# Performance work log

Measured on AMD Instinct MI355X. Metric: run time of the kernel, lower is better.

## Reference

```python
import math
import jax, jax.numpy as jnp
import numpy as np

B, N, C = 2, 2048, 1024
H = 16
D = C // H  # 64
LN_EPS = 1e-5


def setup_inputs() -> dict:
    key = jax.random.key(0)
    ks = jax.random.split(key, 5)
    x = jax.random.normal(ks[0], (B, N, C), dtype=jnp.float32)
    w_qkv = jax.random.normal(ks[1], (C, 3 * C), dtype=jnp.float32) * 0.02
    w_proj = jax.random.normal(ks[2], (C, C), dtype=jnp.float32) * 0.02
    b_proj = jnp.zeros((C,), dtype=jnp.float32)
    ln_w = jnp.ones((D,), dtype=jnp.float32) + jax.random.normal(ks[3], (D,), dtype=jnp.float32) * 0.02
    ln_b = jax.random.normal(ks[4], (D,), dtype=jnp.float32) * 0.02
    return {"x": x, "w_qkv": w_qkv, "w_proj": w_proj, "b_proj": b_proj,
            "ln_w": ln_w, "ln_b": ln_b}


def _layernorm(t, w, b):
    mu = jnp.mean(t, axis=-1, keepdims=True)
    var = jnp.var(t, axis=-1, keepdims=True)
    return (t - mu) * jax.lax.rsqrt(var + LN_EPS) * w + b


def reference(x, w_qkv, w_proj, b_proj, ln_w, ln_b):
    b, n, c = x.shape
    h, d = H, c // H
    # QKV projection (no bias): [b,n,3c] -> [3,b,h,n,d]
    qkv = (x @ w_qkv).reshape(b, n, 3, h, d).transpose(2, 0, 3, 1, 4)
    q, k, v = qkv[0], qkv[1], qkv[2]
    # per-head LayerNorm on q and k (qk_norm)
    q = _layernorm(q, ln_w, ln_b)
    k = _layernorm(k, ln_w, ln_b)
    # NOTE: source multiplies q by sqrt(head_dim) (faithful to original)
    q = q * jnp.asarray(math.sqrt(d), dtype=q.dtype)
    scores = jnp.einsum('bhnd,bhmd->bhnm', q, k)  # [b,h,n,n]
    mask_value = -jnp.finfo(scores.dtype).max
    causal = jnp.tril(jnp.ones((n, n), dtype=bool))
    scores = jnp.where(causal, scores, mask_value)
    attn = jax.nn.softmax(scores, axis=-1)
    out = jnp.einsum('bhnm,bhmd->bhnd', attn, v)  # [b,h,n,d]
    out = out.transpose(0, 2, 1, 3).reshape(b, n, c)  # b n (h d)
    return out @ w_proj + b_proj
```

## Files before the change

kernel.cpp:

```cpp
#include <hip/hip_runtime.h>

#define LOG2E 1.4426950408889634f

typedef _Float16 f16x8_t __attribute__((ext_vector_type(8)));
typedef _Float16 f16x4_t __attribute__((ext_vector_type(4)));
typedef _Float16 f16x2_t __attribute__((ext_vector_type(2)));
typedef float    f32x4_t __attribute__((ext_vector_type(4)));

#define MFMA32(a, b, c) __builtin_amdgcn_mfma_f32_16x16x32_f16(a, b, c, 0, 0, 0)
#define MFMA16(a, b, c) __builtin_amdgcn_mfma_f32_16x16x16f16(a, b, c, 0, 0, 0)

__device__ __forceinline__ void async_copy16(void* lds, const void* g) {
    __builtin_amdgcn_global_load_lds(
        (const __attribute__((address_space(1))) unsigned char*)g,
        (__attribute__((address_space(3))) unsigned char*)lds, 16, 0, 0);
}

__global__ void prep_k(const float* __restrict__ x, _Float16* __restrict__ xh,
                       const float* __restrict__ wq, _Float16* __restrict__ wqT,
                       const float* __restrict__ wp, _Float16* __restrict__ wpT) {
    __shared__ _Float16 tl[64][65];
    const int bx = blockIdx.x, t = threadIdx.x;
    if (bx < 4096) {
        const int i = bx * 256 + t;
        float4 v = ((const float4*)x)[i];
        f16x4_t o = { (_Float16)v.x, (_Float16)v.y, (_Float16)v.z, (_Float16)v.w };
        ((f16x4_t*)xh)[i] = o;
        return;
    }
    const float* in; _Float16* out; int C, bxx, byy;
    if (bx < 4864) { const int id = bx - 4096; in = wq; out = wqT; C = 3072; bxx = id % 48; byy = id / 48; }
    else           { const int id = bx - 4864; in = wp; out = wpT; C = 1024; bxx = id % 16; byy = id / 16; }
    const int R = 1024;
    const int c = t & 63;
    const int r4 = t >> 6;
    const int r0 = byy * 64, c0 = bxx * 64;
#pragma unroll
    for (int i = 0; i < 16; ++i) {
        int r = r4 + i * 4;
        tl[c][r] = (_Float16)in[(size_t)(r0 + r) * C + c0 + c];
    }
    __syncthreads();
#pragma unroll
    for (int i = 0; i < 16; ++i) {
        int rr = r4 + i * 4;
        out[(size_t)(c0 + rr) * R + r0 + c] = tl[rr][c];
    }
}

template <typename OutT, bool BIAS, bool LNQK>
__global__ __launch_bounds__(256, 3)
void gemm_f16_k(const _Float16* __restrict__ A, const _Float16* __restrict__ BT,
                OutT* __restrict__ C, const float* __restrict__ bias,
                _Float16* __restrict__ VTg,
                const float* __restrict__ ln_w, const float* __restrict__ ln_b,
                int M, int N, int K) {
    __shared__ _Float16 As[2][128][32];
    __shared__ _Float16 Bs[2][128][32];
    const int tid = threadIdx.x;
    const int wid = tid >> 6, lane = tid & 63;
    const int qd = lane >> 4, ln = lane & 15;
    const int m0 = blockIdx.x * 128, n0 = blockIdx.y * 128;
    const int wm = (wid >> 1) * 64, wn = (wid & 1) * 64;

    f32x4_t acc[4][4] = {};

    const int srow = lane >> 2;
    const int skk  = (lane & 3) * 8;

    for (int k0 = 0; k0 < K; k0 += 64) {
        __syncthreads();
#pragma unroll
        for (int p = 0; p < 4; ++p) {
            const int seg = p * 4 + wid;
            const int s   = seg >> 3;
            const int rg  = seg & 7;
            const int row = rg * 16 + srow;
            const size_t goff = (size_t)row * K + k0 + s * 32 + skk;
            async_copy16(&As[0][0][0] + seg * 512, A  + (size_t)m0 * K + goff);
            async_copy16(&Bs[0][0][0] + seg * 512, BT + (size_t)n0 * K + goff);
        }
        __syncthreads();
#pragma unroll
        for (int s = 0; s < 2; ++s) {
            f16x8_t a[4], b[4];
#pragma unroll
            for (int i = 0; i < 4; ++i)
                a[i] = *(const f16x8_t*)&As[s][wm + i * 16 + ln][qd * 8];
#pragma unroll
            for (int j = 0; j < 4; ++j)
                b[j] = *(const f16x8_t*)&Bs[s][wn + j * 16 + ln][qd * 8];
#pragma unroll
            for (int i = 0; i < 4; ++i)
#pragma unroll
                for (int j = 0; j < 4; ++j)
                    acc[i][j] = MFMA32(a[i], b[j], acc[i][j]);
        }
    }

    if constexpr (LNQK) {
        if (n0 >= 2048) {
            __syncthreads();
            const int h2  = ((n0 - 2048) >> 6) + (wn >> 6);
            const int row0 = m0 + wm;
            const int bb  = row0 >> 11;
            const int tt  = (row0 & 2047) >> 6;
            const size_t obase = ((size_t)(bb * 16 + h2)) * 131072 + (size_t)tt * 4096;
            _Float16* tlw = &As[0][0][0] + wid * 1088;
#pragma unroll
            for (int j = 0; j < 4; ++j) {
#pragma unroll
                for (int i = 0; i < 4; ++i) {
                    f16x4_t v;
#pragma unroll
                    for (int r = 0; r < 4; ++r) v[r] = (_Float16)acc[i][j][r];
                    *(f16x4_t*)&tlw[ln * 68 + i * 16 + qd * 4] = v;
                }
#pragma unroll
                for (int e = 0; e < 2; ++e) {
                    const int ci = lane * 2 + e;
                    const int dl = ci >> 3, w2 = ci & 7;
                    const int pq = w2 ^ (dl & 7);
                    const int base = (pq >> 2) * 32 + (pq & 3) * 4;
                    f16x4_t v0 = *(const f16x4_t*)&tlw[dl * 68 + base];
                    f16x4_t v1 = *(const f16x4_t*)&tlw[dl * 68 + base + 16];
                    f16x8_t val = __builtin_shufflevector(v0, v1, 0, 1, 2, 3, 4, 5, 6, 7);
                    *(f16x8_t*)&VTg[obase + (size_t)((j * 16 + dl) * 8 + w2) * 8] = val;
                }
            }
            return;
        }
        {
            const float scale = (n0 < 1024) ? 8.0f * LOG2E : 1.0f;
            float lw[4], lb[4];
#pragma unroll
            for (int j = 0; j < 4; ++j) { lw[j] = ln_w[j * 16 + ln]; lb[j] = ln_b[j * 16 + ln]; }
#pragma unroll
            for (int i = 0; i < 4; ++i)
#pragma unroll
                for (int r = 0; r < 4; ++r) {
                    float s = acc[i][0][r] + acc[i][1][r] + acc[i][2][r] + acc[i][3][r];
                    s += __shfl_xor(s, 1); s += __shfl_xor(s, 2);
                    s += __shfl_xor(s, 4); s += __shfl_xor(s, 8);
                    const float mu = s * 0.015625f;
                    const float d0 = acc[i][0][r] - mu, d1 = acc[i][1][r] - mu;
                    const float d2 = acc[i][2][r] - mu, d3 = acc[i][3][r] - mu;
                    float v = d0 * d0 + d1 * d1 + d2 * d2 + d3 * d3;
                    v += __shfl_xor(v, 1); v += __shfl_xor(v, 2);
                    v += __shfl_xor(v, 4); v += __shfl_xor(v, 8);
                    const float rs = rsqrtf(v * 0.015625f + 1e-5f);
                    acc[i][0][r] = (d0 * rs * lw[0] + lb[0]) * scale;
                    acc[i][1][r] = (d1 * rs * lw[1] + lb[1]) * scale;
                    acc[i][2][r] = (d2 * rs * lw[2] + lb[2]) * scale;
                    acc[i][3][r] = (d3 * rs * lw[3] + lb[3]) * scale;
                }
        }
    }

#pragma unroll
    for (int i = 0; i < 4; ++i)
#pragma unroll
        for (int j = 0; j < 4; ++j) {
            const int col = n0 + wn + j * 16 + ln;
            const float bv = BIAS ? bias[col] : 0.0f;
#pragma unroll
            for (int r = 0; r < 4; ++r) {
                const int row = m0 + wm + i * 16 + qd * 4 + r;
                C[(size_t)row * N + col] = (OutT)(acc[i][j][r] + bv);
            }
        }
}

__global__ __launch_bounds__(256, 2)
void gemm_f16_m64_k(const _Float16* __restrict__ A, const _Float16* __restrict__ BT,
                    float* __restrict__ C, const float* __restrict__ bias,
                    int M, int N, int K) {
    __shared__ _Float16 As[2][64][32];
    __shared__ _Float16 Bs[2][128][32];
    const int tid = threadIdx.x;
    const int wid = tid >> 6, lane = tid & 63;
    const int qd = lane >> 4, ln = lane & 15;
    const int m0 = blockIdx.x * 64, n0 = blockIdx.y * 128;
    const int wn = wid * 32;

    f32x4_t acc[4][2] = {};
    const int srow = lane >> 2;
    const int skk  = (lane & 3) * 8;

    for (int k0 = 0; k0 < K; k0 += 64) {
        __syncthreads();
#pragma unroll
        for (int p = 0; p < 2; ++p) {
            const int seg = p * 4 + wid;
            const int hidx = seg * 512 + lane * 8;
            const int s_ = hidx >> 11;
            const int row = (hidx >> 5) & 63;
            const int kk = hidx & 31;
            async_copy16(&As[0][0][0] + seg * 512,
                         A + (size_t)(m0 + row) * K + k0 + s_ * 32 + kk);
        }
#pragma unroll
        for (int p = 0; p < 4; ++p) {
            const int seg = p * 4 + wid;
            const int s   = seg >> 3;
            const int rg  = seg & 7;
            const int row = rg * 16 + srow;
            async_copy16(&Bs[0][0][0] + seg * 512,
                         BT + (size_t)(n0 + row) * K + k0 + s * 32 + skk);
        }
        __syncthreads();
#pragma unroll
        for (int s = 0; s < 2; ++s) {
            f16x8_t a[4], b[2];
#pragma unroll
            for (int i = 0; i < 4; ++i)
                a[i] = *(const f16x8_t*)&As[s][i * 16 + ln][qd * 8];
#pragma unroll
            for (int j = 0; j < 2; ++j)
                b[j] = *(const f16x8_t*)&Bs[s][wn + j * 16 + ln][qd * 8];
#pragma unroll
            for (int i = 0; i < 4; ++i)
#pragma unroll
                for (int j = 0; j < 2; ++j)
                    acc[i][j] = MFMA32(a[i], b[j], acc[i][j]);
        }
    }
#pragma unroll
    for (int i = 0; i < 4; ++i)
#pragma unroll
        for (int j = 0; j < 2; ++j) {
            const int col = n0 + wn + j * 16 + ln;
            const float bv = bias[col];
#pragma unroll
            for (int r = 0; r < 4; ++r) {
                const int row = m0 + i * 16 + qd * 4 + r;
                C[(size_t)row * N + col] = acc[i][j][r] + bv;
            }
        }
}

__global__ __launch_bounds__(256, 3)
void attn_part_k(const _Float16* __restrict__ qkv, const _Float16* __restrict__ VTg,
                 _Float16* __restrict__ O, float* __restrict__ Op, float* __restrict__ ml) {
    __shared__ _Float16 Ks[3][2][64][32];
    __shared__ _Float16 VT[3][64][64];

    const int tid = threadIdx.x;
    const int wid = tid >> 6, lane = tid & 63;
    const int qd = lane >> 4, ln = lane & 15;
    const int bh = blockIdx.x;
    const int b = bh >> 4, h = bh & 15;
    const int y = blockIdx.y;
    int band, chunk, nst;
    if (y < 8)       { band = 8 + y;  chunk = 0; nst = 16; }
    else if (y < 16) { band = 23 - y; chunk = 1; nst = 2 * band - 14; }
    else             { band = y - 16; chunk = 0; nst = 2 * band + 2; }
    const size_t vtbase = (size_t)bh * 131072;
    const int qrow0 = band * 128 + wid * 32;
    const int kvbeg = chunk * 1024;

    f16x8_t qf[2][2];
#pragma unroll
    for (int qt = 0; qt < 2; ++qt)
#pragma unroll
        for (int s = 0; s < 2; ++s)
            qf[qt][s] = *(const f16x8_t*)&qkv[(size_t)(b * 2048 + qrow0 + qt * 16 + ln) * 3072
                                             + h * 64 + s * 32 + qd * 8];

    f32x4_t o[2][4] = {};
    f32x4_t ls[2] = {};
    float m[2] = { -3.0e38f, -3.0e38f };
    const f16x4_t ones = { (_Float16)1.0f, (_Float16)1.0f, (_Float16)1.0f, (_Float16)1.0f };

    auto stage = [&](int buf, int kv0) {
#pragma unroll
        for (int p = 0; p < 2; ++p) {
            const int seg = p * 4 + wid;
            const int hidx = seg * 512 + lane * 8;
            const int s_ = hidx >> 11;
            const int rrow = (hidx >> 5) & 63;
            const int kk = hidx & 31;
            async_copy16(&Ks[buf][0][0][0] + seg * 512,
                         qkv + (size_t)(b * 2048 + kv0 + rrow) * 3072 + 1024 + h * 64
                             + s_ * 32 + kk);
        }
#pragma unroll
        for (int p = 0; p < 2; ++p) {
            const int seg = p * 4 + wid;
            async_copy16(&VT[buf][0][0] + seg * 512,
                         VTg + vtbase + (size_t)kv0 * 64 + seg * 512 + lane * 8);
        }
    };

    stage(0, kvbeg);
    stage(1, kvbeg + 64);

    for (int st = 0; st < nst; ++st) {
        const int kv0 = kvbeg + st * 64;
        if (st + 1 < nst) asm volatile("s_waitcnt vmcnt(4)" ::: "memory");
        else              asm volatile("s_waitcnt vmcnt(0)" ::: "memory");
        __builtin_amdgcn_s_barrier();
        asm volatile("" ::: "memory");
        if (st + 2 < nst) stage((st + 2) % 3, kv0 + 128);
        const int buf = st % 3;

        if (kv0 <= qrow0 + 31) {
            f32x4_t sc[2][4];
#pragma unroll
            for (int jt = 0; jt < 4; ++jt) {
                f16x8_t k0 = *(const f16x8_t*)&Ks[buf][0][jt * 16 + ln][qd * 8];
                f16x8_t k1 = *(const f16x8_t*)&Ks[buf][1][jt * 16 + ln][qd * 8];
#pragma unroll
                for (int qt = 0; qt < 2; ++qt) {
                    f32x4_t s = {};
                    s = MFMA32(k0, qf[qt][0], s);
                    s = MFMA32(k1, qf[qt][1], s);
                    sc[qt][jt] = s;
                }
            }
            f16x8_t vf8[4][2];
#pragma unroll
            for (int dt = 0; dt < 4; ++dt)
#pragma unroll
                for (int pp = 0; pp < 2; ++pp) {
                    const int w = (pp * 4 + qd) ^ (ln & 7);
                    vf8[dt][pp] = *(const f16x8_t*)&VT[buf][dt * 16 + ln][w * 8];
                }

#pragma unroll
            for (int qt = 0; qt < 2; ++qt) {
                if (kv0 + 63 > qrow0 + qt * 16) {
                    const int qq = qrow0 + qt * 16 + ln;
#pragma unroll
                    for (int c = 0; c < 4; ++c)
#pragma unroll
                        for (int r = 0; r < 4; ++r)
                            if (kv0 + c * 16 + qd * 4 + r > qq) sc[qt][c][r] = -3.0e38f;
                }
                float mx0 = fmaxf(fmaxf(fmaxf(sc[qt][0][0], sc[qt][1][0]), sc[qt][2][0]), sc[qt][3][0]);
                float mx1 = fmaxf(fmaxf(fmaxf(sc[qt][0][1], sc[qt][1][1]), sc[qt][2][1]), sc[qt][3][1]);
                float mx2 = fmaxf(fmaxf(fmaxf(sc[qt][0][2], sc[qt][1][2]), sc[qt][2][2]), sc[qt][3][2]);
                float mx3 = fmaxf(fmaxf(fmaxf(sc[qt][0][3], sc[qt][1][3]), sc[qt][2][3]), sc[qt][3][3]);
                float mx = fmaxf(fmaxf(fmaxf(mx0, mx1), mx2), mx3);
                mx = fmaxf(mx, __shfl_xor(mx, 16));
                mx = fmaxf(mx, __shfl_xor(mx, 32));
                if (!__all(mx <= m[qt] + 8.0f)) {
                    const float mn = fmaxf(m[qt], mx);
                    const float al = exp2f(m[qt] - mn);
#pragma unroll
                    for (int dt = 0; dt < 4; ++dt) o[qt][dt] *= al;
                    ls[qt][0] *= al;
                    m[qt] = mn;
                }
                f16x4_t pf[4];
#pragma unroll
                for (int c = 0; c < 4; ++c) {
                    float p0 = exp2f(sc[qt][c][0] - m[qt]);
                    float p1 = exp2f(sc[qt][c][1] - m[qt]);
                    float p2 = exp2f(sc[qt][c][2] - m[qt]);
                    float p3 = exp2f(sc[qt][c][3] - m[qt]);
                    f16x2_t a = __builtin_bit_cast(f16x2_t, __builtin_amdgcn_cvt_pkrtz(p0, p1));
                    f16x2_t bb = __builtin_bit_cast(f16x2_t, __builtin_amdgcn_cvt_pkrtz(p2, p3));
                    pf[c] = __builtin_shufflevector(a, bb, 0, 1, 2, 3);
                }
                __builtin_amdgcn_s_setprio(1);
#pragma unroll
                for (int c = 0; c < 4; ++c) ls[qt] = MFMA16(ones, pf[c], ls[qt]);
#pragma unroll
                for (int dt = 0; dt < 4; ++dt)
#pragma unroll
                    for (int pp = 0; pp < 2; ++pp) {
                        f16x4_t lo = __builtin_shufflevector(vf8[dt][pp], vf8[dt][pp], 0, 1, 2, 3);
                        f16x4_t hi = __builtin_shufflevector(vf8[dt][pp], vf8[dt][pp], 4, 5, 6, 7);
                        o[qt][dt] = MFMA16(lo, pf[pp * 2 + 0], o[qt][dt]);
                        o[qt][dt] = MFMA16(hi, pf[pp * 2 + 1], o[qt][dt]);
                    }
                __builtin_amdgcn_s_setprio(0);
            }
        }
    }

    if (band < 8) {
        const size_t base0 = ((size_t)(b * 2048 + qrow0 + ln)) * 1024 + h * 64 + qd * 4;
#pragma unroll
        for (int qt = 0; qt < 2; ++qt) {
            const float inv = 1.0f / ls[qt][0];
            const size_t base = base0 + (size_t)qt * 16 * 1024;
#pragma unroll
            for (int dt = 0; dt < 4; ++dt) {
                f16x4_t ov;
#pragma unroll
                for (int r = 0; r < 4; ++r) ov[r] = (_Float16)(o[qt][dt][r] * inv);
                *(f16x4_t*)&O[base + dt * 16] = ov;
            }
        }
    } else {
        const size_t pb = ((size_t)bh * 8 + (band - 8)) * 2 + chunk;
#pragma unroll
        for (int qt = 0; qt < 2; ++qt) {
            const int row = wid * 32 + qt * 16 + ln;
            float* op = Op + pb * 8192 + (size_t)row * 64 + qd * 4;
#pragma unroll
            for (int dt = 0; dt < 4; ++dt)
                *(f32x4_t*)&op[dt * 16] = o[qt][dt];
            if (qd == 0) {
                ml[pb * 256 + row * 2]     = m[qt];
                ml[pb * 256 + row * 2 + 1] = ls[qt][0];
            }
        }
    }
}

__global__ __launch_bounds__(256)
void attn_merge_k(const float* __restrict__ Op, const float* __restrict__ ml,
                  _Float16* __restrict__ O) {
    const int bh = blockIdx.x, bnd = blockIdx.y;
    const int b = bh >> 4, h = bh & 15;
    const int band = 8 + bnd;
    const size_t pb = ((size_t)bh * 8 + bnd) * 2;
    const int tid = threadIdx.x;
    const int row = tid >> 1;
    const int c32 = (tid & 1) * 32;
    const float m0 = ml[pb * 256 + row * 2],       l0 = ml[pb * 256 + row * 2 + 1];
    const float m1 = ml[(pb + 1) * 256 + row * 2], l1 = ml[(pb + 1) * 256 + row * 2 + 1];
    const float mm = fmaxf(m0, m1);
    const float a0 = exp2f(m0 - mm), a1 = exp2f(m1 - mm);
    const float inv = 1.0f / (l0 * a0 + l1 * a1);
    const float* p0 = Op + pb * 8192 + (size_t)row * 64 + c32;
    const float* p1 = p0 + 8192;
    _Float16* op = O + ((size_t)(b * 2048 + band * 128 + row)) * 1024 + h * 64 + c32;
#pragma unroll
    for (int g = 0; g < 8; ++g) {
        f32x4_t v0 = *(const f32x4_t*)&p0[g * 4];
        f32x4_t v1 = *(const f32x4_t*)&p1[g * 4];
        f16x4_t ov;
#pragma unroll
        for (int r = 0; r < 4; ++r)
            ov[r] = (_Float16)((v0[r] * a0 + v1[r] * a1) * inv);
        *(f16x4_t*)&op[g * 4] = ov;
    }
}

extern "C" void kernel_launch(void* const* d_in, const int* in_sizes, int n_in,
                              void* d_out, int out_size, void* d_ws, size_t ws_size,
                              hipStream_t stream) {
    const float* x      = (const float*)d_in[0];
    const float* w_qkv  = (const float*)d_in[1];
    const float* w_proj = (const float*)d_in[2];
    const float* b_proj = (const float*)d_in[3];
    const float* ln_w   = (const float*)d_in[4];
    const float* ln_b   = (const float*)d_in[5];
    float* out = (float*)d_out;

    char* w = (char*)d_ws;
    const size_t MB = 1024 * 1024;
    _Float16*  qkv    = (_Float16*)(w);
    _Float16*  xh     = (_Float16*)(w + 24 * MB);
    _Float16*  wqkvT  = (_Float16*)(w + 32 * MB);
    _Float16*  wprojT = (_Float16*)(w + 38 * MB);
    _Float16*  VTg    = (_Float16*)(w + 40 * MB);
    _Float16*  Ah     = (_Float16*)(w + 48 * MB);
    float*     Op     = (float*)(w + 56 * MB);
    float*     mlb    = (float*)(w + 72 * MB);

    prep_k<<<5120, 256, 0, stream>>>(x, xh, w_qkv, wqkvT, w_proj, wprojT);
    gemm_f16_k<_Float16, false, true><<<dim3(32, 24), 256, 0, stream>>>(
        xh, wqkvT, qkv, nullptr, VTg, ln_w, ln_b, 4096, 3072, 1024);
    attn_part_k<<<dim3(32, 24), 256, 0, stream>>>(qkv, VTg, Ah, Op, mlb);
    attn_merge_k<<<dim3(32, 8), 256, 0, stream>>>(Op, mlb, Ah);
    gemm_f16_m64_k<<<dim3(64, 8), 256, 0, stream>>>(Ah, wprojT, out, b_proj, 4096, 1024, 1024);
}
```

Measured before the change: 190.6 us.

## Double-buffer GEMM K-loop with prefetch, XCD-aware block remap, shrink attention buffers

Both f16 GEMM kernels now load tiles 32 wide in K into two LDS buffers. The next tile is issued asynchronously while the current one feeds the MFMAs, instead of loading 64 wide and computing with a barrier between. Workgroup IDs are remapped so that consecutive blocks on the same XCD cover neighbouring tiles, which is meant to improve L2 reuse. The attention kernel drops from triple to double buffering of K/V with a plain __syncthreads, which frees LDS but shortens the prefetch lookahead. The aim is to hide global load latency in the GEMMs, at the cost of more barriers per K step and possibly less latency hiding in attention.

```diff
diff --git a/kernel.cpp b/kernel.cpp
--- a/kernel.cpp
+++ b/kernel.cpp
@@ -60,7 +60,12 @@
     const int tid = threadIdx.x;
     const int wid = tid >> 6, lane = tid & 63;
     const int qd = lane >> 4, ln = lane & 15;
-    const int m0 = blockIdx.x * 128, n0 = blockIdx.y * 128;
+    const int flat = blockIdx.y * gridDim.x + blockIdx.x;
+    const int nwg = gridDim.x * gridDim.y;
+    const int cpx = nwg >> 3;
+    const int nf = (flat & 7) * cpx + (flat >> 3);
+    const int bx = nf / gridDim.y, by = nf % gridDim.y;
+    const int m0 = bx * 128, n0 = by * 128;
     const int wm = (wid >> 1) * 64, wn = (wid & 1) * 64;
 
     f32x4_t acc[4][4] = {};
@@ -68,34 +73,33 @@
     const int srow = lane >> 2;
     const int skk  = (lane & 3) * 8;
 
-    for (int k0 = 0; k0 < K; k0 += 64) {
+    auto stage = [&](int buf, int k0) {
+#pragma unroll
+        for (int p = 0; p < 2; ++p) {
+            const int seg = p * 4 + wid;
+            const int row = seg * 16 + srow;
+            async_copy16(&As[buf][0][0] + seg * 512, A  + (size_t)(m0 + row) * K + k0 + skk);
+            async_copy16(&Bs[buf][0][0] + seg * 512, BT + (size_t)(n0 + row) * K + k0 + skk);
+        }
+    };
+
+    stage(0, 0);
+    for (int k0 = 0; k0 < K; k0 += 32) {
+        const int buf = (k0 >> 5) & 1;
         __syncthreads();
-#pragma unroll
-        for (int p = 0; p < 4; ++p) {
-            const int seg = p * 4 + wid;
-            const int s   = seg >> 3;
-            const int rg  = seg & 7;
-            const int row = rg * 16 + srow;
-            const size_t goff = (size_t)row * K + k0 + s * 32 + skk;
-            async_copy16(&As[0][0][0] + seg * 512, A  + (size_t)m0 * K + goff);
-            async_copy16(&Bs[0][0][0] + seg * 512, BT + (size_t)n0 * K + goff);
-        }
-        __syncthreads();
-#pragma unroll
-        for (int s = 0; s < 2; ++s) {
-            f16x8_t a[4], b[4];
-#pragma unroll
-            for (int i = 0; i < 4; ++i)
-                a[i] = *(const f16x8_t*)&As[s][wm + i * 16 + ln][qd * 8];
+        if (k0 + 32 < K) stage(buf ^ 1, k0 + 32);
+        f16x8_t a[4], b[4];
+#pragma unroll
+        for (int i = 0; i < 4; ++i)
+            a[i] = *(const f16x8_t*)&As[buf][wm + i * 16 + ln][qd * 8];
+#pragma unroll
+        for (int j = 0; j < 4; ++j)
+            b[j] = *(const f16x8_t*)&Bs[buf][wn + j * 16 + ln][qd * 8];
+#pragma unroll
+        for (int i = 0; i < 4; ++i)
 #pragma unroll
             for (int j = 0; j < 4; ++j)
-                b[j] = *(const f16x8_t*)&Bs[s][wn + j * 16 + ln][qd * 8];
-#pragma unroll
-            for (int i = 0; i < 4; ++i)
-#pragma unroll
-                for (int j = 0; j < 4; ++j)
-                    acc[i][j] = MFMA32(a[i], b[j], acc[i][j]);
-        }
+                acc[i][j] = MFMA32(a[i], b[j], acc[i][j]);
     }
 
     if constexpr (LNQK) {
@@ -180,50 +184,48 @@
     const int tid = threadIdx.x;
     const int wid = tid >> 6, lane = tid & 63;
     const int qd = lane >> 4, ln = lane & 15;
-    const int m0 = blockIdx.x * 64, n0 = blockIdx.y * 128;
+    const int flat = blockIdx.y * gridDim.x + blockIdx.x;
+    const int nwg = gridDim.x * gridDim.y;
+    const int cpx = nwg >> 3;
+    const int nf = (flat & 7) * cpx + (flat >> 3);
+    const int bx = nf / gridDim.y, by = nf % gridDim.y;
+    const int m0 = bx * 64, n0 = by * 128;
     const int wn = wid * 32;
 
     f32x4_t acc[4][2] = {};
     const int srow = lane >> 2;
     const int skk  = (lane & 3) * 8;
 
-    for (int k0 = 0; k0 < K; k0 += 64) {
-        __syncthreads();
+    auto stage = [&](int buf, int k0) {
+        {
+            const int row = wid * 16 + srow;
+            async_copy16(&As[buf][0][0] + wid * 512, A + (size_t)(m0 + row) * K + k0 + skk);
+        }
 #pragma unroll
         for (int p = 0; p < 2; ++p) {
             const int seg = p * 4 + wid;
-            const int hidx = seg * 512 + lane * 8;
-            const int s_ = hidx >> 11;
-            const int row = (hidx >> 5) & 63;
-            const int kk = hidx & 31;
-            async_copy16(&As[0][0][0] + seg * 512,
-                         A + (size_t)(m0 + row) * K + k0 + s_ * 32 + kk);
-        }
-#pragma unroll
-        for (int p = 0; p < 4; ++p) {
-            const int seg = p * 4 + wid;
-            const int s   = seg >> 3;
-            const int rg  = seg & 7;
-            const int row = rg * 16 + srow;
-            async_copy16(&Bs[0][0][0] + seg * 512,
-                         BT + (size_t)(n0 + row) * K + k0 + s * 32 + skk);
-        }
+            const int row = seg * 16 + srow;
+            async_copy16(&Bs[buf][0][0] + seg * 512, BT + (size_t)(n0 + row) * K + k0 + skk);
+        }
+    };
+
+    stage(0, 0);
+    for (int k0 = 0; k0 < K; k0 += 32) {
+        const int buf = (k0 >> 5) & 1;
         __syncthreads();
-#pragma unroll
-        for (int s = 0; s < 2; ++s) {
-            f16x8_t a[4], b[2];
-#pragma unroll
-            for (int i = 0; i < 4; ++i)
-                a[i] = *(const f16x8_t*)&As[s][i * 16 + ln][qd * 8];
+        if (k0 + 32 < K) stage(buf ^ 1, k0 + 32);
+        f16x8_t a[4], b[2];
+#pragma unroll
+        for (int i = 0; i < 4; ++i)
+            a[i] = *(const f16x8_t*)&As[buf][i * 16 + ln][qd * 8];
+#pragma unroll
+        for (int j = 0; j < 2; ++j)
+            b[j] = *(const f16x8_t*)&Bs[buf][wn + j * 16 + ln][qd * 8];
+#pragma unroll
+        for (int i = 0; i < 4; ++i)
 #pragma unroll
             for (int j = 0; j < 2; ++j)
-                b[j] = *(const f16x8_t*)&Bs[s][wn + j * 16 + ln][qd * 8];
-#pragma unroll
-            for (int i = 0; i < 4; ++i)
-#pragma unroll
-                for (int j = 0; j < 2; ++j)
-                    acc[i][j] = MFMA32(a[i], b[j], acc[i][j]);
-        }
+                acc[i][j] = MFMA32(a[i], b[j], acc[i][j]);
     }
 #pragma unroll
     for (int i = 0; i < 4; ++i)
@@ -242,8 +244,8 @@
 __global__ __launch_bounds__(256, 3)
 void attn_part_k(const _Float16* __restrict__ qkv, const _Float16* __restrict__ VTg,
                  _Float16* __restrict__ O, float* __restrict__ Op, float* __restrict__ ml) {
-    __shared__ _Float16 Ks[3][2][64][32];
-    __shared__ _Float16 VT[3][64][64];
+    __shared__ _Float16 Ks[2][2][64][32];
+    __shared__ _Float16 VT[2][64][64];
 
     const int tid = threadIdx.x;
     const int wid = tid >> 6, lane = tid & 63;
@@ -293,16 +295,12 @@
     };
 
     stage(0, kvbeg);
-    stage(1, kvbeg + 64);
 
     for (int st = 0; st < nst; ++st) {
         const int kv0 = kvbeg + st * 64;
-        if (st + 1 < nst) asm volatile("s_waitcnt vmcnt(4)" ::: "memory");
-        else              asm volatile("s_waitcnt vmcnt(0)" ::: "memory");
-        __builtin_amdgcn_s_barrier();
-        asm volatile("" ::: "memory");
-        if (st + 2 < nst) stage((st + 2) % 3, kv0 + 128);
-        const int buf = st % 3;
+        __syncthreads();
+        if (st + 1 < nst) stage((st + 1) & 1, kv0 + 64);
+        const int buf = st & 1;
 
         if (kv0 <= qrow0 + 31) {
             f32x4_t sc[2][4];
```

New measurement: 197.8 us. 1.04x slower.
